# Kernel tuning notes

Measured on AMD Instinct MI355X. Metric: run time of the kernel, lower is better.

The kernel has to match this reference:

```python
import jax, jax.numpy as jnp
import numpy as np


def _forward(q, k, Wq, bq, Wk, bk, Wp, bp, eps=1e-4):
    b, ck, hk, wk, dk = k.shape
    n = hk * wk * dk                      # k sequence length == per-block q tokens
    # k branch: flatten spatial, project 256 -> 32
    kf = jnp.einsum('bci,cd->bid', k.reshape(b, ck, n), Wk) + bk   # (b, n, C)
    k_norm = jnp.linalg.norm(kf, axis=1)                           # (b, C): norm over positions (torch dim=1)
    c = q.shape[1]
    hq, wq, dq = q.shape[2], q.shape[3], q.shape[4]
    Nq = hq * wq * dq
    qf = jnp.einsum('bci,cd->bid', q.reshape(b, c, Nq), Wq) + bq   # (b, Nq, C)
    C = qf.shape[-1]
    Bh, Bw, Bd = hq // hk, wq // wk, dq // dk
    G = Bh * Bw * Bd
    # gather all (h_k, w_k, d_k) blocks: (b, G, n, C) -- replaces triple python loop
    qb = (qf.reshape(b, Bh, hk, Bw, wk, Bd, dk, C)
            .transpose(0, 1, 3, 5, 2, 4, 6, 7)
            .reshape(b, G, n, C))
    q_norm = jnp.linalg.norm(qb, axis=2)                           # (b, G, C): per-channel norm over block positions
    denom = jnp.einsum('bc,bgc->bg', k_norm, q_norm) + eps         # scalar per (batch, block)
    # sim[b,g,j,i] = <kf[b,i,:], qb[b,g,j,:]> / denom  (already in post-permute layout)
    sim = jnp.einsum('bic,bgjc->bgji', kf, qb) / denom[:, :, None, None]
    att = jax.nn.softmax(sim, axis=-1)                             # softmax over k positions i
    out = jnp.einsum('bgji,bgic->bgjc', att, qb)                   # (b, G, n, C)
    # min-max renorm over positions within each block (torch dim=1 of (b,n,C))
    mn = out.min(axis=2, keepdims=True)
    mx = out.max(axis=2, keepdims=True)
    v = (out - mn) / (mx - mn + eps)
    # faithful torch reshape: (b, C, n) row-major reinterpreted as (b, hk, wk, dk, C)
    v = v.transpose(0, 1, 3, 2).reshape(b, Bh, Bw, Bd, hk, wk, dk, C)
    # scatter blocks back to full volume
    v = v.transpose(0, 1, 4, 2, 5, 3, 6, 7).reshape(b, hq, wq, dq, C)
    out = jnp.einsum('bhwdc,ce->bhwde', v, Wp) + bp
    return out.transpose(0, 4, 1, 2, 3)                            # (b, C, hq, wq, dq)


def setup_inputs() -> dict:
    key = jax.random.key(0)
    ks = jax.random.split(key, 8)
    nf = 16
    q = jax.random.normal(ks[0], (2, nf * 2, 32, 32, 32), jnp.float32)
    k = jax.random.normal(ks[1], (2, nf * 16, 8, 8, 8), jnp.float32)
    Wq = jax.random.normal(ks[2], (nf * 2, nf * 2), jnp.float32) * 0.05
    bq = jax.random.normal(ks[3], (nf * 2,), jnp.float32) * 0.05
    Wk = jax.random.normal(ks[4], (nf * 16, nf * 2), jnp.float32) * 0.05
    bk = jax.random.normal(ks[5], (nf * 2,), jnp.float32) * 0.05
    Wp = jax.random.normal(ks[6], (nf * 2, nf * 2), jnp.float32) * 0.05
    bp = jax.random.normal(ks[7], (nf * 2,), jnp.float32) * 0.05
    return {"q": q, "k": k, "Wq": Wq, "bq": bq, "Wk": Wk, "bk": bk, "Wp": Wp, "bp": bp}


def reference(q, k, Wq, bq, Wk, bk, Wp, bp):
    return _forward(q, k, Wq, bq, Wk, bk, Wp, bp)
```

## Files before the change

kernel.cpp:

```cpp
#include <hip/hip_runtime.h>
#include <hip/hip_bf16.h>
#include <cstdint>

typedef __attribute__((ext_vector_type(8))) short bf16x8;
typedef __attribute__((ext_vector_type(4))) float f32x4;

static __device__ __forceinline__ float lo16(uint32_t u){ return __uint_as_float(u << 16); }
static __device__ __forceinline__ float hi16(uint32_t u){ return __uint_as_float(u & 0xffff0000u); }
static __device__ __forceinline__ uint32_t f2bf(float x){
    uint32_t u = __float_as_uint(x);
    return (u + 0x7fffu + ((u >> 16) & 1u)) >> 16;
}
static __device__ __forceinline__ uint32_t pack2(float a, float b){
    return f2bf(a) | (f2bf(b) << 16);
}

__global__ __launch_bounds__(256) void k_kf(const float* __restrict__ k,
    const float* __restrict__ Wk, const float* __restrict__ bk,
    uint32_t* __restrict__ kf_pack)
{
    __shared__ float Wk_s[256*32];
    __shared__ float bk_s[32];
    int t = threadIdx.x;
    for (int L = t; L < 8192; L += 256) Wk_s[L] = Wk[L];
    if (t < 32) bk_s[t] = bk[t];
    __syncthreads();
    int blk = blockIdx.x;
    int b = blk >> 7, i0 = (blk & 127) * 4;
    int d = t & 31, sub = t >> 5;
    int i = i0 + (sub >> 1);
    int chalf = sub & 1;
    const float* kb = k + (size_t)b * 131072;
    float acc = chalf ? 0.f : bk_s[d];
    #pragma unroll 8
    for (int cc = 0; cc < 128; ++cc){
        int c = chalf*128 + cc;
        acc += kb[c*512 + i] * Wk_s[c*32 + d];
    }
    acc += __shfl_xor(acc, 32, 64);
    float accO = __shfl_xor(acc, 1, 64);
    if (chalf == 0 && (d & 1) == 0)
        kf_pack[(b*512 + i)*16 + (d >> 1)] = pack2(acc, accO);
}

__global__ __launch_bounds__(256) void k_qb(const float* __restrict__ q,
    const float* __restrict__ Wq, const float* __restrict__ bq,
    uint32_t* __restrict__ qb_pack)
{
    __shared__ float Wq_s[1024], bq_s[32], q_s[8192];
    int t = threadIdx.x;
    int blk = blockIdx.x;
    int bg = blk >> 1, h = blk & 1;
    int b = bg >> 6, g = bg & 63;
    int bh = g >> 4, bw = (g >> 2) & 3, bd = g & 3;
    for (int L = t; L < 1024; L += 256) Wq_s[L] = Wq[L];
    if (t < 32) bq_s[t] = bq[t];
    const float* qbase = q + (size_t)b * 1048576;
    #pragma unroll
    for (int m = 0; m < 8; ++m){
        int L4 = m*256 + t;
        int f4 = L4 & 1, iw = (L4 >> 1) & 7, ihl = (L4 >> 4) & 3, c = L4 >> 6;
        const float* src = qbase + c*32768 + (bh*8 + h*4 + ihl)*1024
                         + (bw*8 + iw)*32 + bd*8 + f4*4;
        float4 v = *(const float4*)src;
        *(float4*)&q_s[c*256 + ihl*64 + iw*8 + f4*4] = v;
    }
    __syncthreads();
    int d = t & 31, sub = t >> 5;
    uint32_t* qb_out = qb_pack + (size_t)bg * 8192 + h*4096;
    for (int it = 0; it < 32; ++it){
        int jl = it*8 + sub;
        float acc = bq_s[d];
        #pragma unroll
        for (int c = 0; c < 32; ++c)
            acc += q_s[c*256 + jl] * Wq_s[c*32 + d];
        float accO = __shfl_xor(acc, 1, 64);
        if ((d & 1) == 0) qb_out[jl*16 + (d >> 1)] = pack2(acc, accO);
    }
}

__global__ __launch_bounds__(256) void k_attn_mfma(const uint32_t* __restrict__ kf_pack,
    const uint32_t* __restrict__ qb_pack,
    float* __restrict__ oraw, float* __restrict__ mnp, float* __restrict__ mxp)
{
    __shared__ uint32_t kfs32[8192];
    __shared__ uint16_t qbV16[16384];
    __shared__ uint16_t Ps16[4096];
    __shared__ float mred[4][4][64];
    __shared__ float stat[16][32];
    __shared__ float dens[4][16];
    __shared__ float knsh[32], vssh[32], dsh[32];
    __shared__ float denom_s;
    int t = threadIdx.x;
    int blk = blockIdx.x;
    int bg = blk >> 1, jhalf = blk & 1;
    int b = bg >> 6;
    {
        const uint32_t* src = kf_pack + b*8192;
        for (int m = 0; m < 32; ++m){
            int flat = m*256 + t;
            uint32_t v = src[flat];
            int i = flat >> 4, dp = flat & 15;
            kfs32[i*16 + (((dp>>2) ^ (i&3)) & 3)*4 + (dp&3)] = v;
        }
    }
    {
        const uint32_t* src = qb_pack + (size_t)bg*8192;
        for (int m = 0; m < 32; ++m){
            int flat = m*256 + t;
            int i = flat >> 4, dp = flat & 15;
            uint32_t v = src[flat];
            int d0 = 2*dp, d1 = 2*dp + 1;
            qbV16[d0*512 + (((i>>3) ^ (d0&7)) & 63)*8 + (i&7)] = (uint16_t)(v & 0xffffu);
            qbV16[d1*512 + (((i>>3) ^ (d1&7)) & 63)*8 + (i&7)] = (uint16_t)(v >> 16);
        }
    }
    __syncthreads();
    {
        int dp = t & 15, ig = t >> 4;
        float lo2 = 0.f, hi2 = 0.f;
        #pragma unroll 8
        for (int ii = 0; ii < 32; ++ii){
            int i = ig*32 + ii;
            uint32_t u = kfs32[i*16 + (((dp>>2) ^ (i&3)) & 3)*4 + (dp&3)];
            float a = lo16(u), c = hi16(u);
            lo2 += a*a; hi2 += c*c;
        }
        stat[ig][dp*2] = lo2; stat[ig][dp*2+1] = hi2;
    }
    __syncthreads();
    if (t < 32){
        float s = 0.f;
        #pragma unroll
        for (int u = 0; u < 16; ++u) s += stat[u][t];
        knsh[t] = s;
    }
    __syncthreads();
    {
        int d = t & 31, ig = t >> 5;
        float q2 = 0.f, vs = 0.f;
        #pragma unroll 8
        for (int ii = 0; ii < 64; ii += 2){
            int i = ig*64 + ii;
            uint32_t u = *(__shared__ uint32_t*)&qbV16[d*512 + (((i>>3) ^ (d&7)) & 63)*8 + (i&7)];
            float a = lo16(u), c = hi16(u);
            q2 += a*a + c*c; vs += a + c;
        }
        stat[ig][d] = q2; stat[8 + ig][d] = vs;
    }
    __syncthreads();
    if (t < 32){
        float q2 = 0.f, vs = 0.f;
        #pragma unroll
        for (int u = 0; u < 8; ++u){ q2 += stat[u][t]; vs += stat[8+u][t]; }
        vssh[t] = vs;
        dsh[t] = sqrtf(knsh[t]) * sqrtf(q2);
    }
    __syncthreads();
    if (t == 0){
        float s = 0.f;
        #pragma unroll
        for (int d2 = 0; d2 < 32; ++d2) s += dsh[d2];
        denom_s = s + 1e-4f;
    }
    __syncthreads();
    float rden = 1.0f / denom_s;
    int wave = t >> 6, lane = t & 63;
    int ln15 = lane & 15, quad = lane >> 4;
    uint16_t* Pw = Ps16 + wave*1024;
    float vs0[4], vs1[4];
    #pragma unroll
    for (int r = 0; r < 4; ++r){
        vs0[r] = vssh[quad*4 + r];
        vs1[r] = vssh[16 + quad*4 + r];
    }
    float* obase = oraw + (size_t)bg * 16384;
    for (int jt = 0; jt < 4; ++jt){
        int jloc = (wave*4 + jt)*16 + ln15;
        int jglob = jhalf*256 + jloc;
        union { bf16x8 v; uint16_t u[8]; } afr;
        #pragma unroll
        for (int jj = 0; jj < 8; ++jj){
            int d = quad*8 + jj;
            afr.u[jj] = qbV16[d*512 + (((jglob>>3) ^ (d&7)) & 63)*8 + (jglob&7)];
        }
        f32x4 pv0 = {0.f,0.f,0.f,0.f}, pv1 = {0.f,0.f,0.f,0.f};
        float pdn[4] = {0.f,0.f,0.f,0.f};
        for (int sb = 0; sb < 4; ++sb){
            f32x4 sacc[8];
            #pragma unroll
            for (int u = 0; u < 8; ++u){
                int i = sb*128 + u*16 + ln15;
                bf16x8 bfr = *(__shared__ bf16x8*)&kfs32[i*16 + ((quad ^ (i&3)) & 3)*4];
                f32x4 z = {0.f,0.f,0.f,0.f};
                sacc[u] = __builtin_amdgcn_mfma_f32_16x16x32_bf16(afr.v, bfr, z, 0, 0, 0);
            }
            #pragma unroll
            for (int h2 = 0; h2 < 2; ++h2){
                #pragma unroll
                for (int u4 = 0; u4 < 4; ++u4){
                    int u = h2*4 + u4;
                    int il = u4*16 + ln15;
                    #pragma unroll
                    for (int r = 0; r < 4; ++r){
                        float x = sacc[u][r] * rden;
                        float e = x + x*x*(0.5f + x*(1.0f/6.0f));
                        pdn[r] += e;
                        int jrow = quad*4 + r;
                        Pw[jrow*64 + (((il>>3) ^ (jrow&3)) & 7)*8 + (il&7)] = (uint16_t)f2bf(e);
                    }
                }
                __threadfence_block();
                #pragma unroll
                for (int ks = 0; ks < 2; ++ks){
                    int i0 = ks*32 + quad*8;
                    bf16x8 bp = *(__shared__ bf16x8*)&Pw[ln15*64 + (((i0>>3) ^ (ln15&3)) & 7)*8];
                    int ig = sb*128 + h2*64 + i0;
                    int c0 = ln15, c1 = 16 + ln15;
                    bf16x8 av0 = *(__shared__ bf16x8*)&qbV16[c0*512 + (((ig>>3) ^ (c0&7)) & 63)*8];
                    bf16x8 av1 = *(__shared__ bf16x8*)&qbV16[c1*512 + (((ig>>3) ^ (c1&7)) & 63)*8];
                    pv0 = __builtin_amdgcn_mfma_f32_16x16x32_bf16(av0, bp, pv0, 0, 0, 0);
                    pv1 = __builtin_amdgcn_mfma_f32_16x16x32_bf16(av1, bp, pv1, 0, 0, 0);
                }
            }
        }
        #pragma unroll
        for (int r = 0; r < 4; ++r){
            float s = pdn[r];
            s += __shfl_xor(s, 1, 64);
            s += __shfl_xor(s, 2, 64);
            s += __shfl_xor(s, 4, 64);
            s += __shfl_xor(s, 8, 64);
            if (ln15 == 0) dens[wave][quad*4 + r] = s;
        }
        __threadfence_block();
        float rl = 1.0f / (512.f + dens[wave][ln15]);
        float o0[4], o1[4];
        #pragma unroll
        for (int r = 0; r < 4; ++r){
            o0[r] = (vs0[r] + pv0[r]) * rl;
            o1[r] = (vs1[r] + pv1[r]) * rl;
            obase[(quad*4 + r)*512 + jglob]      = o0[r];
            obase[(16 + quad*4 + r)*512 + jglob] = o1[r];
        }
        #pragma unroll
        for (int r = 0; r < 4; ++r){
            float mnA = o0[r], mxA = o0[r], mnB = o1[r], mxB = o1[r];
            #pragma unroll
            for (int off = 1; off < 16; off <<= 1){
                mnA = fminf(mnA, __shfl_xor(mnA, off, 64));
                mxA = fmaxf(mxA, __shfl_xor(mxA, off, 64));
                mnB = fminf(mnB, __shfl_xor(mnB, off, 64));
                mxB = fmaxf(mxB, __shfl_xor(mxB, off, 64));
            }
            if (ln15 == 0){
                mred[wave][jt][quad*4 + r]      = mnA;
                mred[wave][jt][32 + quad*4 + r] = mxA;
                mred[wave][jt][16 + quad*4 + r]      = mnB;
                mred[wave][jt][48 + quad*4 + r] = mxB;
            }
        }
        __threadfence_block();
    }
    __syncthreads();
    if (t < 32){
        float mn = 3e38f, mx = -3e38f;
        #pragma unroll
        for (int w = 0; w < 4; ++w)
            #pragma unroll
            for (int j2 = 0; j2 < 4; ++j2){
                mn = fminf(mn, mred[w][j2][t]);
                mx = fmaxf(mx, mred[w][j2][32 + t]);
            }
        int slot = (bg*2 + jhalf)*32 + t;
        mnp[slot] = mn;
        mxp[slot] = mx;
    }
}

__global__ __launch_bounds__(256) void k_proj(const float* __restrict__ oraw,
    const float* __restrict__ mnp, const float* __restrict__ mxp,
    const float* __restrict__ Wp, const float* __restrict__ bp,
    float* __restrict__ out)
{
    __shared__ float Wp_s[1024], bp_s[32];
    __shared__ float sh_v[32][32];
    __shared__ float sh_o[32][33];
    int t = threadIdx.x;
    if (t < 32) bp_s[t] = bp[t];
    for (int L = t; L < 1024; L += 256) Wp_s[L] = Wp[L];
    int blk = blockIdx.x;
    int b = blk >> 10, p0 = (blk & 1023) * 32;
    int c = t & 31, ip0 = t >> 5;
    float vv[4];
    #pragma unroll
    for (int m = 0; m < 4; ++m){
        int p = p0 + m*8 + ip0;
        int h = p >> 10, w = (p >> 5) & 31, dsp = p & 31;
        int f = (h >> 3)*262144 + (w >> 3)*65536 + (dsp >> 3)*16384
              + (h & 7)*2048 + (w & 7)*256 + (dsp & 7)*32;
        int flat = f + c;
        int cidx = b*2048 + (flat >> 9);
        int s0 = ((cidx >> 5) << 6) + (cidx & 31);
        float o  = oraw[(size_t)b*1048576 + flat];
        float mn = fminf(mnp[s0], mnp[s0 + 32]);
        float mx = fmaxf(mxp[s0], mxp[s0 + 32]);
        vv[m] = (o - mn) / (mx - mn + 1e-4f);
    }
    __syncthreads();
    #pragma unroll
    for (int m = 0; m < 4; ++m) sh_v[m*8 + ip0][c] = vv[m];
    __syncthreads();
    #pragma unroll
    for (int m = 0; m < 4; ++m){
        int pos = m*8 + ip0;
        float acc = bp_s[c];
        #pragma unroll
        for (int cc = 0; cc < 32; ++cc)
            acc += sh_v[pos][cc] * Wp_s[cc*32 + c];
        sh_o[pos][c] = acc;
    }
    __syncthreads();
    #pragma unroll
    for (int m = 0; m < 4; ++m){
        int e = m*8 + (t >> 5), pi = t & 31;
        out[((size_t)(b*32 + e) << 15) + p0 + pi] = sh_o[pi][e];
    }
}

extern "C" void kernel_launch(void* const* d_in, const int* in_sizes, int n_in,
                              void* d_out, int out_size, void* d_ws, size_t ws_size,
                              hipStream_t stream)
{
    const float* q  = (const float*)d_in[0];
    const float* k  = (const float*)d_in[1];
    const float* Wq = (const float*)d_in[2];
    const float* bq = (const float*)d_in[3];
    const float* Wk = (const float*)d_in[4];
    const float* bk = (const float*)d_in[5];
    const float* Wp = (const float*)d_in[6];
    const float* bp = (const float*)d_in[7];

    float* base      = (float*)d_ws;
    uint32_t* kf_pack = (uint32_t*)base;
    uint32_t* qb_pack = (uint32_t*)(base + 16384);
    float* oraw      = base + 1064960;
    float* mnp       = base + 3162112;
    float* mxp       = base + 3170304;
    float* outp      = (float*)d_out;

    hipLaunchKernelGGL(k_kf,        dim3(256),  dim3(256), 0, stream, k, Wk, bk, kf_pack);
    hipLaunchKernelGGL(k_qb,        dim3(256),  dim3(256), 0, stream, q, Wq, bq, qb_pack);
    hipLaunchKernelGGL(k_attn_mfma, dim3(256),  dim3(256), 0, stream, kf_pack, qb_pack, oraw, mnp, mxp);
    hipLaunchKernelGGL(k_proj,      dim3(2048), dim3(256), 0, stream, oraw, mnp, mxp, Wp, bp, outp);
}
```

Baseline: 136.1 us.

## Quadruple block size to 1024 threads in kf, qb and attention kernels

Raises the first three kernels from 256 to 1024 threads per block while keeping the grid at 256 blocks. Each thread now does a quarter of the work: in the attention kernel each wave handles one 16-row tile instead of looping over four, and the kf projection splits the channel reduction eight ways with a shared-memory reduction step. This aims to raise per-CU parallelism on a grid that is too small to fill the GPU. In exchange it needs more LDS per block (Ps16, stat, red) and tighter register limits under 1024-thread launch bounds, which may cause spills or reduce how many blocks fit per CU.

```diff
diff --git a/kernel.cpp b/kernel.cpp
--- a/kernel.cpp
+++ b/kernel.cpp
@@ -15,35 +15,43 @@
     return f2bf(a) | (f2bf(b) << 16);
 }
 
-__global__ __launch_bounds__(256) void k_kf(const float* __restrict__ k,
+__global__ __launch_bounds__(1024) void k_kf(const float* __restrict__ k,
     const float* __restrict__ Wk, const float* __restrict__ bk,
     uint32_t* __restrict__ kf_pack)
 {
-    __shared__ float Wk_s[256*32];
+    __shared__ float Wk_s[8192];
     __shared__ float bk_s[32];
+    __shared__ float red[32][32];
     int t = threadIdx.x;
-    for (int L = t; L < 8192; L += 256) Wk_s[L] = Wk[L];
+    for (int L = t; L < 8192; L += 1024) Wk_s[L] = Wk[L];
     if (t < 32) bk_s[t] = bk[t];
     __syncthreads();
     int blk = blockIdx.x;
     int b = blk >> 7, i0 = (blk & 127) * 4;
     int d = t & 31, sub = t >> 5;
-    int i = i0 + (sub >> 1);
-    int chalf = sub & 1;
+    int i = i0 + (sub >> 3);
+    int cp = sub & 7;
     const float* kb = k + (size_t)b * 131072;
-    float acc = chalf ? 0.f : bk_s[d];
+    float acc = 0.f;
     #pragma unroll 8
-    for (int cc = 0; cc < 128; ++cc){
-        int c = chalf*128 + cc;
+    for (int cc = 0; cc < 32; ++cc){
+        int c = cp*32 + cc;
         acc += kb[c*512 + i] * Wk_s[c*32 + d];
     }
-    acc += __shfl_xor(acc, 32, 64);
-    float accO = __shfl_xor(acc, 1, 64);
-    if (chalf == 0 && (d & 1) == 0)
-        kf_pack[(b*512 + i)*16 + (d >> 1)] = pack2(acc, accO);
-}
-
-__global__ __launch_bounds__(256) void k_qb(const float* __restrict__ q,
+    red[sub][d] = acc;
+    __syncthreads();
+    if (t < 128){
+        int isel = t >> 5, dd = t & 31;
+        float s = bk_s[dd];
+        #pragma unroll
+        for (int cp2 = 0; cp2 < 8; ++cp2) s += red[isel*8 + cp2][dd];
+        float sO = __shfl_xor(s, 1, 64);
+        if ((dd & 1) == 0)
+            kf_pack[(b*512 + i0 + isel)*16 + (dd >> 1)] = pack2(s, sO);
+    }
+}
+
+__global__ __launch_bounds__(1024) void k_qb(const float* __restrict__ q,
     const float* __restrict__ Wq, const float* __restrict__ bq,
     uint32_t* __restrict__ qb_pack)
 {
@@ -53,12 +61,12 @@
     int bg = blk >> 1, h = blk & 1;
     int b = bg >> 6, g = bg & 63;
     int bh = g >> 4, bw = (g >> 2) & 3, bd = g & 3;
-    for (int L = t; L < 1024; L += 256) Wq_s[L] = Wq[L];
+    Wq_s[t & 1023] = Wq[t & 1023];
     if (t < 32) bq_s[t] = bq[t];
     const float* qbase = q + (size_t)b * 1048576;
     #pragma unroll
-    for (int m = 0; m < 8; ++m){
-        int L4 = m*256 + t;
+    for (int m = 0; m < 2; ++m){
+        int L4 = m*1024 + t;
         int f4 = L4 & 1, iw = (L4 >> 1) & 7, ihl = (L4 >> 4) & 3, c = L4 >> 6;
         const float* src = qbase + c*32768 + (bh*8 + h*4 + ihl)*1024
                          + (bw*8 + iw)*32 + bd*8 + f4*4;
@@ -68,8 +76,8 @@
     __syncthreads();
     int d = t & 31, sub = t >> 5;
     uint32_t* qb_out = qb_pack + (size_t)bg * 8192 + h*4096;
-    for (int it = 0; it < 32; ++it){
-        int jl = it*8 + sub;
+    for (int it = 0; it < 8; ++it){
+        int jl = it*32 + sub;
         float acc = bq_s[d];
         #pragma unroll
         for (int c = 0; c < 32; ++c)
@@ -79,16 +87,16 @@
     }
 }
 
-__global__ __launch_bounds__(256) void k_attn_mfma(const uint32_t* __restrict__ kf_pack,
+__global__ __launch_bounds__(1024) void k_attn_mfma(const uint32_t* __restrict__ kf_pack,
     const uint32_t* __restrict__ qb_pack,
     float* __restrict__ oraw, float* __restrict__ mnp, float* __restrict__ mxp)
 {
     __shared__ uint32_t kfs32[8192];
     __shared__ uint16_t qbV16[16384];
-    __shared__ uint16_t Ps16[4096];
-    __shared__ float mred[4][4][64];
-    __shared__ float stat[16][32];
-    __shared__ float dens[4][16];
+    __shared__ uint16_t Ps16[16384];
+    __shared__ float mred[16][64];
+    __shared__ float stat[64][32];
+    __shared__ float dens[16][16];
     __shared__ float knsh[32], vssh[32], dsh[32];
     __shared__ float denom_s;
     int t = threadIdx.x;
@@ -97,8 +105,9 @@
     int b = bg >> 6;
     {
         const uint32_t* src = kf_pack + b*8192;
-        for (int m = 0; m < 32; ++m){
-            int flat = m*256 + t;
+        #pragma unroll
+        for (int m = 0; m < 8; ++m){
+            int flat = m*1024 + t;
             uint32_t v = src[flat];
             int i = flat >> 4, dp = flat & 15;
             kfs32[i*16 + (((dp>>2) ^ (i&3)) & 3)*4 + (dp&3)] = v;
@@ -106,8 +115,9 @@
     }
     {
         const uint32_t* src = qb_pack + (size_t)bg*8192;
-        for (int m = 0; m < 32; ++m){
-            int flat = m*256 + t;
+        #pragma unroll
+        for (int m = 0; m < 8; ++m){
+            int flat = m*1024 + t;
             int i = flat >> 4, dp = flat & 15;
             uint32_t v = src[flat];
             int d0 = 2*dp, d1 = 2*dp + 1;
@@ -119,9 +129,9 @@
     {
         int dp = t & 15, ig = t >> 4;
         float lo2 = 0.f, hi2 = 0.f;
-        #pragma unroll 8
-        for (int ii = 0; ii < 32; ++ii){
-            int i = ig*32 + ii;
+        #pragma unroll
+        for (int ii = 0; ii < 8; ++ii){
+            int i = ig*8 + ii;
             uint32_t u = kfs32[i*16 + (((dp>>2) ^ (i&3)) & 3)*4 + (dp&3)];
             float a = lo16(u), c = hi16(u);
             lo2 += a*a; hi2 += c*c;
@@ -132,27 +142,27 @@
     if (t < 32){
         float s = 0.f;
         #pragma unroll
-        for (int u = 0; u < 16; ++u) s += stat[u][t];
+        for (int u = 0; u < 64; ++u) s += stat[u][t];
         knsh[t] = s;
     }
     __syncthreads();
     {
         int d = t & 31, ig = t >> 5;
         float q2 = 0.f, vs = 0.f;
-        #pragma unroll 8
-        for (int ii = 0; ii < 64; ii += 2){
-            int i = ig*64 + ii;
+        #pragma unroll
+        for (int ii = 0; ii < 16; ii += 2){
+            int i = ig*16 + ii;
             uint32_t u = *(__shared__ uint32_t*)&qbV16[d*512 + (((i>>3) ^ (d&7)) & 63)*8 + (i&7)];
             float a = lo16(u), c = hi16(u);
             q2 += a*a + c*c; vs += a + c;
         }
-        stat[ig][d] = q2; stat[8 + ig][d] = vs;
+        stat[ig][d] = q2; stat[32 + ig][d] = vs;
     }
     __syncthreads();
     if (t < 32){
         float q2 = 0.f, vs = 0.f;
         #pragma unroll
-        for (int u = 0; u < 8; ++u){ q2 += stat[u][t]; vs += stat[8+u][t]; }
+        for (int u = 0; u < 32; ++u){ q2 += stat[u][t]; vs += stat[32+u][t]; }
         vssh[t] = vs;
         dsh[t] = sqrtf(knsh[t]) * sqrtf(q2);
     }
@@ -175,103 +185,98 @@
         vs1[r] = vssh[16 + quad*4 + r];
     }
     float* obase = oraw + (size_t)bg * 16384;
-    for (int jt = 0; jt < 4; ++jt){
-        int jloc = (wave*4 + jt)*16 + ln15;
-        int jglob = jhalf*256 + jloc;
-        union { bf16x8 v; uint16_t u[8]; } afr;
-        #pragma unroll
-        for (int jj = 0; jj < 8; ++jj){
-            int d = quad*8 + jj;
-            afr.u[jj] = qbV16[d*512 + (((jglob>>3) ^ (d&7)) & 63)*8 + (jglob&7)];
-        }
-        f32x4 pv0 = {0.f,0.f,0.f,0.f}, pv1 = {0.f,0.f,0.f,0.f};
-        float pdn[4] = {0.f,0.f,0.f,0.f};
-        for (int sb = 0; sb < 4; ++sb){
-            f32x4 sacc[8];
+    int jloc = wave*16 + ln15;
+    int jglob = jhalf*256 + jloc;
+    union { bf16x8 v; uint16_t u[8]; } afr;
+    #pragma unroll
+    for (int jj = 0; jj < 8; ++jj){
+        int d = quad*8 + jj;
+        afr.u[jj] = qbV16[d*512 + (((jglob>>3) ^ (d&7)) & 63)*8 + (jglob&7)];
+    }
+    f32x4 pv0 = {0.f,0.f,0.f,0.f}, pv1 = {0.f,0.f,0.f,0.f};
+    float pdn[4] = {0.f,0.f,0.f,0.f};
+    for (int sb = 0; sb < 4; ++sb){
+        f32x4 sacc[8];
+        #pragma unroll
+        for (int u = 0; u < 8; ++u){
+            int i = sb*128 + u*16 + ln15;
+            bf16x8 bfr = *(__shared__ bf16x8*)&kfs32[i*16 + ((quad ^ (i&3)) & 3)*4];
+            f32x4 z = {0.f,0.f,0.f,0.f};
+            sacc[u] = __builtin_amdgcn_mfma_f32_16x16x32_bf16(afr.v, bfr, z, 0, 0, 0);
+        }
+        #pragma unroll
+        for (int h2 = 0; h2 < 2; ++h2){
             #pragma unroll
-            for (int u = 0; u < 8; ++u){
-                int i = sb*128 + u*16 + ln15;
-                bf16x8 bfr = *(__shared__ bf16x8*)&kfs32[i*16 + ((quad ^ (i&3)) & 3)*4];
-                f32x4 z = {0.f,0.f,0.f,0.f};
-                sacc[u] = __builtin_amdgcn_mfma_f32_16x16x32_bf16(afr.v, bfr, z, 0, 0, 0);
-            }
-            #pragma unroll
-            for (int h2 = 0; h2 < 2; ++h2){
+            for (int u4 = 0; u4 < 4; ++u4){
+                int u = h2*4 + u4;
+                int il = u4*16 + ln15;
                 #pragma unroll
-                for (int u4 = 0; u4 < 4; ++u4){
-                    int u = h2*4 + u4;
-                    int il = u4*16 + ln15;
-                    #pragma unroll
-                    for (int r = 0; r < 4; ++r){
-                        float x = sacc[u][r] * rden;
-                        float e = x + x*x*(0.5f + x*(1.0f/6.0f));
-                        pdn[r] += e;
-                        int jrow = quad*4 + r;
-                        Pw[jrow*64 + (((il>>3) ^ (jrow&3)) & 7)*8 + (il&7)] = (uint16_t)f2bf(e);
-                    }
-                }
-                __threadfence_block();
-                #pragma unroll
-                for (int ks = 0; ks < 2; ++ks){
-                    int i0 = ks*32 + quad*8;
-                    bf16x8 bp = *(__shared__ bf16x8*)&Pw[ln15*64 + (((i0>>3) ^ (ln15&3)) & 7)*8];
-                    int ig = sb*128 + h2*64 + i0;
-                    int c0 = ln15, c1 = 16 + ln15;
-                    bf16x8 av0 = *(__shared__ bf16x8*)&qbV16[c0*512 + (((ig>>3) ^ (c0&7)) & 63)*8];
-                    bf16x8 av1 = *(__shared__ bf16x8*)&qbV16[c1*512 + (((ig>>3) ^ (c1&7)) & 63)*8];
-                    pv0 = __builtin_amdgcn_mfma_f32_16x16x32_bf16(av0, bp, pv0, 0, 0, 0);
-                    pv1 = __builtin_amdgcn_mfma_f32_16x16x32_bf16(av1, bp, pv1, 0, 0, 0);
+                for (int r = 0; r < 4; ++r){
+                    float x = sacc[u][r] * rden;
+                    float e = x + x*x*(0.5f + x*(1.0f/6.0f));
+                    pdn[r] += e;
+                    int jrow = quad*4 + r;
+                    Pw[jrow*64 + (((il>>3) ^ (jrow&3)) & 7)*8 + (il&7)] = (uint16_t)f2bf(e);
                 }
             }
-        }
-        #pragma unroll
-        for (int r = 0; r < 4; ++r){
-            float s = pdn[r];
-            s += __shfl_xor(s, 1, 64);
-            s += __shfl_xor(s, 2, 64);
-            s += __shfl_xor(s, 4, 64);
-            s += __shfl_xor(s, 8, 64);
-            if (ln15 == 0) dens[wave][quad*4 + r] = s;
-        }
-        __threadfence_block();
-        float rl = 1.0f / (512.f + dens[wave][ln15]);
-        float o0[4], o1[4];
-        #pragma unroll
-        for (int r = 0; r < 4; ++r){
-            o0[r] = (vs0[r] + pv0[r]) * rl;
-            o1[r] = (vs1[r] + pv1[r]) * rl;
-            obase[(quad*4 + r)*512 + jglob]      = o0[r];
-            obase[(16 + quad*4 + r)*512 + jglob] = o1[r];
-        }
-        #pragma unroll
-        for (int r = 0; r < 4; ++r){
-            float mnA = o0[r], mxA = o0[r], mnB = o1[r], mxB = o1[r];
+            __threadfence_block();
             #pragma unroll
-            for (int off = 1; off < 16; off <<= 1){
-                mnA = fminf(mnA, __shfl_xor(mnA, off, 64));
-                mxA = fmaxf(mxA, __shfl_xor(mxA, off, 64));
-                mnB = fminf(mnB, __shfl_xor(mnB, off, 64));
-                mxB = fmaxf(mxB, __shfl_xor(mxB, off, 64));
+            for (int ks = 0; ks < 2; ++ks){
+                int i0 = ks*32 + quad*8;
+                bf16x8 bp = *(__shared__ bf16x8*)&Pw[ln15*64 + (((i0>>3) ^ (ln15&3)) & 7)*8];
+                int ig = sb*128 + h2*64 + i0;
+                int c0 = ln15, c1 = 16 + ln15;
+                bf16x8 av0 = *(__shared__ bf16x8*)&qbV16[c0*512 + (((ig>>3) ^ (c0&7)) & 63)*8];
+                bf16x8 av1 = *(__shared__ bf16x8*)&qbV16[c1*512 + (((ig>>3) ^ (c1&7)) & 63)*8];
+                pv0 = __builtin_amdgcn_mfma_f32_16x16x32_bf16(av0, bp, pv0, 0, 0, 0);
+                pv1 = __builtin_amdgcn_mfma_f32_16x16x32_bf16(av1, bp, pv1, 0, 0, 0);
             }
-            if (ln15 == 0){
-                mred[wave][jt][quad*4 + r]      = mnA;
-                mred[wave][jt][32 + quad*4 + r] = mxA;
-                mred[wave][jt][16 + quad*4 + r]      = mnB;
-                mred[wave][jt][48 + quad*4 + r] = mxB;
-            }
-        }
-        __threadfence_block();
+        }
+    }
+    #pragma unroll
+    for (int r = 0; r < 4; ++r){
+        float s = pdn[r];
+        s += __shfl_xor(s, 1, 64);
+        s += __shfl_xor(s, 2, 64);
+        s += __shfl_xor(s, 4, 64);
+        s += __shfl_xor(s, 8, 64);
+        if (ln15 == 0) dens[wave][quad*4 + r] = s;
+    }
+    __threadfence_block();
+    float rl = 1.0f / (512.f + dens[wave][ln15]);
+    float o0[4], o1[4];
+    #pragma unroll
+    for (int r = 0; r < 4; ++r){
+        o0[r] = (vs0[r] + pv0[r]) * rl;
+        o1[r] = (vs1[r] + pv1[r]) * rl;
+        obase[(quad*4 + r)*512 + jglob]      = o0[r];
+        obase[(16 + quad*4 + r)*512 + jglob] = o1[r];
+    }
+    #pragma unroll
+    for (int r = 0; r < 4; ++r){
+        float mnA = o0[r], mxA = o0[r], mnB = o1[r], mxB = o1[r];
+        #pragma unroll
+        for (int off = 1; off < 16; off <<= 1){
+            mnA = fminf(mnA, __shfl_xor(mnA, off, 64));
+            mxA = fmaxf(mxA, __shfl_xor(mxA, off, 64));
+            mnB = fminf(mnB, __shfl_xor(mnB, off, 64));
+            mxB = fmaxf(mxB, __shfl_xor(mxB, off, 64));
+        }
+        if (ln15 == 0){
+            mred[wave][quad*4 + r]      = mnA;
+            mred[wave][32 + quad*4 + r] = mxA;
+            mred[wave][16 + quad*4 + r] = mnB;
+            mred[wave][48 + quad*4 + r] = mxB;
+        }
     }
     __syncthreads();
     if (t < 32){
         float mn = 3e38f, mx = -3e38f;
         #pragma unroll
-        for (int w = 0; w < 4; ++w)
-            #pragma unroll
-            for (int j2 = 0; j2 < 4; ++j2){
-                mn = fminf(mn, mred[w][j2][t]);
-                mx = fmaxf(mx, mred[w][j2][32 + t]);
-            }
+        for (int w = 0; w < 16; ++w){
+            mn = fminf(mn, mred[w][t]);
+            mx = fmaxf(mx, mred[w][32 + t]);
+        }
         int slot = (bg*2 + jhalf)*32 + t;
         mnp[slot] = mn;
         mxp[slot] = mx;
@@ -349,8 +354,8 @@
     float* mxp       = base + 3170304;
     float* outp      = (float*)d_out;
 
-    hipLaunchKernelGGL(k_kf,        dim3(256),  dim3(256), 0, stream, k, Wk, bk, kf_pack);
-    hipLaunchKernelGGL(k_qb,        dim3(256),  dim3(256), 0, stream, q, Wq, bq, qb_pack);
-    hipLaunchKernelGGL(k_attn_mfma, dim3(256),  dim3(256), 0, stream, kf_pack, qb_pack, oraw, mnp, mxp);
+    hipLaunchKernelGGL(k_kf,        dim3(256),  dim3(1024), 0, stream, k, Wk, bk, kf_pack);
+    hipLaunchKernelGGL(k_qb,        dim3(256),  dim3(1024), 0, stream, q, Wq, bq, qb_pack);
+    hipLaunchKernelGGL(k_attn_mfma, dim3(256),  dim3(1024), 0, stream, kf_pack, qb_pack, oraw, mnp, mxp);
     hipLaunchKernelGGL(k_proj,      dim3(2048), dim3(256), 0, stream, oraw, mnp, mxp, Wp, bp, outp);
 }
```

Result: faster. 127.4 us (-6.4%).
